# Performance work log

Hardware: AMD Instinct MI355X
Metric: run time of the kernel (lower is better)

## Reference

```python
import jax, jax.numpy as jnp
import numpy as np


def setup_inputs() -> dict:
    key = jax.random.key(0)
    ks = jax.random.split(key, 8)
    B, S, V, E, H = 64, 512, 50257, 512, 1024
    scale1 = 1.0 / np.sqrt(E + H)
    scale2 = 1.0 / np.sqrt(H + E)
    return {
        "sequence": jax.random.randint(ks[0], (B, S), 0, V, dtype=jnp.int64),
        "init_h1": jax.random.uniform(ks[1], (B, H), jnp.float32, -0.1, 0.1),
        "init_h2": jax.random.uniform(ks[2], (B, E), jnp.float32, -0.1, 0.1),
        "emb_W": jax.random.normal(ks[3], (V, E), jnp.float32) * 0.02,
        "W1": jax.random.normal(ks[4], (E + H, H), jnp.float32) * scale1,
        "b1": jnp.zeros((H,), jnp.float32),
        "W2": jax.random.normal(ks[5], (H + E, E), jnp.float32) * scale2,
        "b2": jnp.zeros((E,), jnp.float32),
        "out_b": jnp.zeros((V,), jnp.float32),
    }


def reference(sequence, init_h1, init_h2, emb_W, W1, b1, W2, b2, out_b):
    # embeddings: [B, S, E] -> scan over time axis
    emb = emb_W[sequence]  # gather, [B, S, E]
    emb_t = jnp.swapaxes(emb, 0, 1)  # [S, B, E]

    def step(carry, token):
        h1, h2 = carry  # [B,H], [B,E]
        in1 = jnp.concatenate([token, h1], axis=1)  # [B, E+H]
        new_h1 = jnp.tanh(in1 @ W1 + b1)            # [B, H]
        in2 = jnp.concatenate([new_h1, h2], axis=1)  # [B, H+E]
        new_h2 = jnp.tanh(in2 @ W2 + b2)             # [B, E]
        return (new_h1, new_h2), None

    (h1, h2), _ = jax.lax.scan(step, (init_h1, init_h2), emb_t)
    # tied output projection: Linear with weight = embedding table [V, E]
    probabilities = h2 @ emb_W.T + out_b  # [B, V]
    return probabilities, h1, h2
```

## Files before the change

### kernel.cpp

```cpp
#include <hip/hip_runtime.h>
#include <hip/hip_bf16.h>

#define BB 64
#define EE 512
#define HH 1024
#define KK 1536
#define VV 50257
#define SS 512

#define NWG1 64
#define NWG2 32
#define NWG (NWG1 + NWG2)
#define RING 64
#define PADU 32

typedef __bf16 bf16x8 __attribute__((ext_vector_type(8)));
typedef float f32x4 __attribute__((ext_vector_type(4)));

__device__ __forceinline__ bf16x8 load_bf8(const __bf16* p) {
    return *reinterpret_cast<const bf16x8*>(p);
}

__device__ __forceinline__ bf16x8 cvt8(const float* p) {
    f32x4 a = *reinterpret_cast<const f32x4*>(p);
    f32x4 b = *reinterpret_cast<const f32x4*>(p + 4);
    bf16x8 r;
    r[0] = (__bf16)a[0]; r[1] = (__bf16)a[1]; r[2] = (__bf16)a[2]; r[3] = (__bf16)a[3];
    r[4] = (__bf16)b[0]; r[5] = (__bf16)b[1]; r[6] = (__bf16)b[2]; r[7] = (__bf16)b[3];
    return r;
}

__device__ __forceinline__ void st16c(void* p, f32x4 v) {
    asm volatile("global_store_dwordx4 %0, %1, off sc0 sc1" :: "v"(p), "v"(v) : "memory");
}
__device__ __forceinline__ f32x4 ld16c(const void* p) {
    f32x4 r;
    asm volatile("global_load_dwordx4 %0, %1, off sc0 sc1" : "=v"(r) : "v"(p) : "memory");
    return r;
}
union cvu { f32x4 f; bf16x8 h8; __bf16 h[8]; };

__device__ __forceinline__ void block_wait(const unsigned* slots, int nslots,
                                           unsigned target) {
    if (threadIdx.x < 64) {
        const int l = threadIdx.x;
        const int idx = l < nslots ? l : 0;
        for (;;) {
            unsigned v = __hip_atomic_load(&slots[idx * PADU], __ATOMIC_RELAXED,
                                           __HIP_MEMORY_SCOPE_AGENT);
            if (l >= nslots) v = target;
            if (__all((int)(v >= target))) break;
            __builtin_amdgcn_s_sleep(1);
        }
    }
    __syncthreads();
    asm volatile("" ::: "memory");
}

__device__ __forceinline__ unsigned minpoll(const unsigned* slots, int nslots) {
    const int l = threadIdx.x & 63;
    unsigned v = 0xFFFFFFFFu;
    if (l < nslots)
        v = __hip_atomic_load(&slots[l * PADU], __ATOMIC_RELAXED,
                              __HIP_MEMORY_SCOPE_AGENT);
    #pragma unroll
    for (int o = 32; o; o >>= 1) {
        unsigned u = (unsigned)__shfl_xor((int)v, o, 64);
        v = u < v ? u : v;
    }
    return v;
}

__device__ __forceinline__ void bsignal(unsigned* slot, unsigned val) {
    asm volatile("s_waitcnt vmcnt(0)" ::: "memory");
    __syncthreads();
    if (threadIdx.x == 0)
        __hip_atomic_store(slot, val, __ATOMIC_RELAXED, __HIP_MEMORY_SCOPE_AGENT);
}

__device__ __forceinline__ float ftanh(float x) {
    float ax = fabsf(x);
    float e = __expf(-2.0f * ax);
    float r = (1.0f - e) / (1.0f + e);
    return x < 0.0f ? -r : r;
}

__global__ void tokens_kernel(const void* __restrict__ seq, int* __restrict__ tok,
                              unsigned* __restrict__ bar) {
    int z = blockIdx.x * 256 + threadIdx.x;
    if (z < 4 * 32 * PADU)
        __hip_atomic_store(&bar[z], 0u, __ATOMIC_RELAXED, __HIP_MEMORY_SCOPE_AGENT);
    const unsigned* u = (const unsigned*)seq;
    bool is64 = true;
    #pragma unroll 1
    for (int i = 0; i < 64; ++i) {
        if (u[2 * i + 1] != 0u) { is64 = false; break; }
    }
    int i = blockIdx.x * 256 + threadIdx.x;
    if (i < BB * SS) tok[i] = is64 ? (int)u[2 * i] : (int)u[i];
}

__global__ __launch_bounds__(256) void transpose_kernel(
    const float* __restrict__ in, __bf16* __restrict__ out, int R, int C) {
    __shared__ float t[32][33];
    int bc = C >> 5;
    int br = blockIdx.x / bc;
    int bco = blockIdx.x % bc;
    int R0 = br << 5, C0 = bco << 5;
    int c = threadIdx.x & 31, r0 = threadIdx.x >> 5;
    #pragma unroll
    for (int i = 0; i < 4; ++i) {
        int r = r0 + i * 8;
        t[r][c] = in[(size_t)(R0 + r) * C + C0 + c];
    }
    __syncthreads();
    #pragma unroll
    for (int i = 0; i < 4; ++i) {
        int r = r0 + i * 8;
        out[(size_t)(C0 + r) * R + R0 + c] = (__bf16)t[c][r];
    }
}

__global__ void init_kernel(const float* __restrict__ h1, const float* __restrict__ h2,
                            __bf16* __restrict__ h1bf, __bf16* __restrict__ h2bf) {
    int i = blockIdx.x * 256 + threadIdx.x;
    if (i < BB * HH) h1bf[i] = (__bf16)h1[i];
    if (i < BB * EE) h2bf[i] = (__bf16)h2[i];
}

__global__ __launch_bounds__(256, 1) void rnn_persist6(
    const int* __restrict__ tok32, const float* __restrict__ embW,
    const float* __restrict__ b1, const float* __restrict__ b2,
    const __bf16* __restrict__ W1t, const __bf16* __restrict__ W2t,
    __bf16* __restrict__ h1r, __bf16* __restrict__ h2r,
    float* __restrict__ h1out, float* __restrict__ h2out,
    unsigned* __restrict__ bar) {
    const int bid = blockIdx.x;
    const bool g1 = bid < NWG1;
    const int rb = g1 ? bid : bid - NWG1;
    const int mi = rb & 3;
    const int ni = rb >> 2;
    const int m0 = mi << 4;
    const int n0 = ni << 6;
    const int tid = threadIdx.x;
    const int w = tid >> 6;
    const int l = tid & 63;
    const int l16 = l & 15;
    const int kg = l >> 4;
    unsigned* f1s = bar + mi * (32 * PADU);
    unsigned* f2s = f1s + 16 * PADU;
    unsigned* myf = g1 ? &f1s[ni * PADU] : &f2s[ni * PADU];

    __shared__ int tok_s[SS][16];
    __shared__ float red[2][4][16][68];

    if (g1) {
        for (int idx = tid; idx < SS * 16; idx += 256) {
            int t = idx >> 4, r = idx & 15;
            tok_s[t][r] = tok32[(m0 + r) * SS + t];
        }
    }

    const __bf16* Wt = g1 ? W1t : W2t;
    bf16x8 wreg[12][4];
    #pragma unroll
    for (int t = 0; t < 12; ++t) {
        const int kb = 32 * (w + 4 * t) + kg * 8;
        #pragma unroll
        for (int nf = 0; nf < 4; ++nf)
            wreg[t][nf] = load_bf8(Wt + (size_t)(n0 + nf * 16 + l16) * KK + kb);
    }
    {
        f32x4* p1 = reinterpret_cast<f32x4*>(&wreg[0][0]);
        #pragma unroll
        for (int q = 0; q < 48; ++q) asm volatile("" : "+v"(p1[q]));
    }

    const int r1 = 4 * w + ((l & 31) >> 3);
    const int c1 = (l & 7) * 8;
    const float* bias = g1 ? b1 : b2;
    const f32x4 blo = *reinterpret_cast<const f32x4*>(bias + n0 + c1);
    const f32x4 bhi = *reinterpret_cast<const f32x4*>(bias + n0 + c1 + 4);

    unsigned f2c = 0;

    __syncthreads();

    if (g1) {
        for (int i = 0; i < SS; ++i) {
            const __bf16* h1i = h1r + (size_t)(i & (RING - 1)) * BB * HH;
            __bf16*       h1n = h1r + (size_t)((i + 1) & (RING - 1)) * BB * HH;

            f32x4 acc[4] = {{0,0,0,0},{0,0,0,0},{0,0,0,0},{0,0,0,0}};
            const float* er = embW + (size_t)tok_s[i][l16] * EE;
            #pragma unroll
            for (int t = 0; t < 4; ++t) {
                bf16x8 ae = cvt8(er + 32 * (w + 4 * t) + kg * 8);
                #pragma unroll
                for (int nf = 0; nf < 4; ++nf)
                    acc[nf] = __builtin_amdgcn_mfma_f32_16x16x32_bf16(
                        ae, wreg[t][nf], acc[nf], 0, 0, 0);
            }
            __builtin_amdgcn_sched_barrier(0);

            if (i >= RING - 1 && (int)f2c < i - (RING - 1)) {
                do { f2c = minpoll(f2s, 8); } while ((int)f2c < i - (RING - 1));
            }

            if (i) block_wait(f1s, 16, (unsigned)i);

            const __bf16* h1row = h1i + (m0 + l16) * HH;
            bf16x8 ah[8];
            #pragma unroll
            for (int u = 0; u < 8; ++u) {
                cvu t_; t_.f = ld16c(h1row + 32 * (w + 4 * u) + kg * 8);
                ah[u] = t_.h8;
            }
            asm volatile("s_waitcnt vmcnt(0)" ::: "memory");
            __builtin_amdgcn_sched_barrier(0);

            #pragma unroll
            for (int u = 0; u < 8; ++u)
                #pragma unroll
                for (int nf = 0; nf < 4; ++nf)
                    acc[nf] = __builtin_amdgcn_mfma_f32_16x16x32_bf16(
                        ah[u], wreg[u + 4][nf], acc[nf], 0, 0, 0);

            #pragma unroll
            for (int nf = 0; nf < 4; ++nf)
                #pragma unroll
                for (int q = 0; q < 4; ++q)
                    red[i & 1][w][kg * 4 + q][nf * 16 + l16] = acc[nf][q];
            __syncthreads();

            if ((l & 63) < 32) {
                f32x4 lo = blo, hi = bhi;
                #pragma unroll
                for (int p = 0; p < 4; ++p) {
                    lo += *reinterpret_cast<const f32x4*>(&red[i & 1][p][r1][c1]);
                    hi += *reinterpret_cast<const f32x4*>(&red[i & 1][p][r1][c1 + 4]);
                }
                cvu o;
                #pragma unroll
                for (int j = 0; j < 4; ++j) {
                    o.h[j]     = (__bf16)ftanh(lo[j]);
                    o.h[j + 4] = (__bf16)ftanh(hi[j]);
                }
                st16c(h1n + (m0 + r1) * HH + n0 + c1, o.f);
                if (i == SS - 1) {
                    float* op = h1out + (m0 + r1) * HH + n0 + c1;
                    #pragma unroll
                    for (int j = 0; j < 8; ++j)
                        op[j] = __bfloat162float(((__hip_bfloat16*)&o.h[j])[0]);
                }
            }
            bsignal(myf, (unsigned)(i + 1));
        }
    } else {
        for (int j = 1; j <= SS; ++j) {
            const __bf16* h1j = h1r + (size_t)(j & (RING - 1)) * BB * HH;
            const __bf16* h2p = h2r + (size_t)((j - 1) & (RING - 1)) * BB * EE;
            __bf16*       h2n = h2r + (size_t)(j & (RING - 1)) * BB * EE;

            block_wait(f1s, 16, (unsigned)j);
            const __bf16* h1row = h1j + (m0 + l16) * HH;
            bf16x8 ah[8];
            #pragma unroll
            for (int t = 0; t < 8; ++t) {
                cvu t_; t_.f = ld16c(h1row + 32 * (w + 4 * t) + kg * 8);
                ah[t] = t_.h8;
            }
            if (j >= 2) block_wait(f2s, 8, (unsigned)(j - 1));
            const __bf16* h2row = h2p + (m0 + l16) * EE;
            bf16x8 a2[4];
            #pragma unroll
            for (int u = 0; u < 4; ++u) {
                cvu t_; t_.f = ld16c(h2row + 32 * (w + 4 * u) + kg * 8);
                a2[u] = t_.h8;
            }
            asm volatile("s_waitcnt vmcnt(0)" ::: "memory");
            __builtin_amdgcn_sched_barrier(0);

            f32x4 acc[4] = {{0,0,0,0},{0,0,0,0},{0,0,0,0},{0,0,0,0}};
            #pragma unroll
            for (int t = 0; t < 8; ++t)
                #pragma unroll
                for (int nf = 0; nf < 4; ++nf)
                    acc[nf] = __builtin_amdgcn_mfma_f32_16x16x32_bf16(
                        ah[t], wreg[t][nf], acc[nf], 0, 0, 0);
            #pragma unroll
            for (int u = 0; u < 4; ++u)
                #pragma unroll
                for (int nf = 0; nf < 4; ++nf)
                    acc[nf] = __builtin_amdgcn_mfma_f32_16x16x32_bf16(
                        a2[u], wreg[u + 8][nf], acc[nf], 0, 0, 0);

            #pragma unroll
            for (int nf = 0; nf < 4; ++nf)
                #pragma unroll
                for (int q = 0; q < 4; ++q)
                    red[j & 1][w][kg * 4 + q][nf * 16 + l16] = acc[nf][q];
            __syncthreads();

            if ((l & 63) < 32) {
                f32x4 lo = blo, hi = bhi;
                #pragma unroll
                for (int p = 0; p < 4; ++p) {
                    lo += *reinterpret_cast<const f32x4*>(&red[j & 1][p][r1][c1]);
                    hi += *reinterpret_cast<const f32x4*>(&red[j & 1][p][r1][c1 + 4]);
                }
                cvu o;
                #pragma unroll
                for (int q = 0; q < 4; ++q) {
                    o.h[q]     = (__bf16)ftanh(lo[q]);
                    o.h[q + 4] = (__bf16)ftanh(hi[q]);
                }
                st16c(h2n + (m0 + r1) * EE + n0 + c1, o.f);
                if (j == SS) {
                    float* op = h2out + (m0 + r1) * EE + n0 + c1;
                    #pragma unroll
                    for (int q = 0; q < 8; ++q)
                        op[q] = __bfloat162float(((__hip_bfloat16*)&o.h[q])[0]);
                }
            }
            bsignal(myf, (unsigned)j);
        }
    }
}

__global__ __launch_bounds__(256) void step_kernel(
    const int* __restrict__ tok32,
    const float* __restrict__ embW,
    const float* __restrict__ b1, const float* __restrict__ b2,
    const __bf16* __restrict__ W1t, const __bf16* __restrict__ W2t,
    const __bf16* __restrict__ h1cur, __bf16* __restrict__ h1next,
    const __bf16* __restrict__ h2cur, __bf16* __restrict__ h2next,
    float* __restrict__ h1f32, float* __restrict__ h2f32,
    int t, int g1, int g2) {
    const int bid = blockIdx.x;
    const bool is1 = bid < 128;
    if (is1 ? (g1 == 0) : (g2 == 0)) return;
    const int rb = is1 ? bid : (bid - 128);
    const int mi = rb & 3;
    const int ni = rb >> 2;
    const int m0 = mi << 4;
    const int n0 = ni << 5;
    const int N = is1 ? HH : EE;
    const int tid = threadIdx.x;
    const int w = tid >> 6;
    const int l = tid & 63;
    const int l16 = l & 15;
    const int kg = l >> 4;

    __shared__ int tok_s[16];
    __shared__ float red[4][16][33];

    if (is1 && tid < 16) tok_s[tid] = tok32[(m0 + tid) * SS + t];
    __syncthreads();

    const __bf16* Wt = is1 ? W1t : W2t;
    f32x4 acc0 = {0.f, 0.f, 0.f, 0.f};
    f32x4 acc1 = {0.f, 0.f, 0.f, 0.f};
    const int row = m0 + l16;
    const int kb = w * 384;

    #pragma unroll 4
    for (int kk = 0; kk < 384; kk += 32) {
        const int k = kb + kk + kg * 8;
        bf16x8 a;
        if (is1) {
            if (k < EE) a = cvt8(embW + (size_t)tok_s[l16] * EE + k);
            else        a = load_bf8(h1cur + row * HH + (k - EE));
        } else {
            if (k < HH) a = load_bf8(h1cur + row * HH + k);
            else        a = load_bf8(h2cur + row * EE + (k - HH));
        }
        bf16x8 bf0 = load_bf8(Wt + (size_t)(n0 + l16) * KK + k);
        bf16x8 bf1 = load_bf8(Wt + (size_t)(n0 + 16 + l16) * KK + k);
        acc0 = __builtin_amdgcn_mfma_f32_16x16x32_bf16(a, bf0, acc0, 0, 0, 0);
        acc1 = __builtin_amdgcn_mfma_f32_16x16x32_bf16(a, bf1, acc1, 0, 0, 0);
    }

    #pragma unroll
    for (int i = 0; i < 4; ++i) {
        red[w][kg * 4 + i][l16]      = acc0[i];
        red[w][kg * 4 + i][16 + l16] = acc1[i];
    }
    __syncthreads();

    const float* bias = is1 ? b1 : b2;
    for (int c = tid; c < 512; c += 256) {
        int m = c >> 5, n = c & 31;
        float s = red[0][m][n] + red[1][m][n] + red[2][m][n] + red[3][m][n];
        s = tanhf(s + bias[n0 + n]);
        int gi = (m0 + m) * N + (n0 + n);
        if (is1) {
            h1next[gi] = (__bf16)s;
            if (h1f32) h1f32[gi] = s;
        } else {
            h2next[gi] = (__bf16)s;
            if (h2f32) h2f32[gi] = s;
        }
    }
}

__global__ __launch_bounds__(256) void proj_kernel(
    const __bf16* __restrict__ h2bf,
    const float* __restrict__ embW,
    const float* __restrict__ outb,
    float* __restrict__ out) {
    const int v0 = blockIdx.x << 6;
    const int tid = threadIdx.x;
    const int w = tid >> 6;
    const int l = tid & 63;
    const int l16 = l & 15, kg = l >> 4;
    const int vcol = v0 + w * 16 + l16;
    const int vr = vcol < VV ? vcol : VV - 1;
    f32x4 acc[4] = {{0,0,0,0},{0,0,0,0},{0,0,0,0},{0,0,0,0}};
    #pragma unroll 2
    for (int k0 = 0; k0 < EE; k0 += 32) {
        const int k = k0 + kg * 8;
        bf16x8 bfr = cvt8(embW + (size_t)vr * EE + k);
        #pragma unroll
        for (int mf = 0; mf < 4; ++mf) {
            bf16x8 a = load_bf8(h2bf + (mf * 16 + l16) * EE + k);
            acc[mf] = __builtin_amdgcn_mfma_f32_16x16x32_bf16(a, bfr, acc[mf], 0, 0, 0);
        }
    }
    if (vcol < VV) {
        const float bb = outb[vcol];
        #pragma unroll
        for (int mf = 0; mf < 4; ++mf) {
            #pragma unroll
            for (int i = 0; i < 4; ++i) {
                int b = mf * 16 + kg * 4 + i;
                out[(size_t)b * VV + vcol] = acc[mf][i] + bb;
            }
        }
    }
}

extern "C" void kernel_launch(void* const* d_in, const int* in_sizes, int n_in,
                              void* d_out, int out_size, void* d_ws, size_t ws_size,
                              hipStream_t stream) {
    const void* seq      = d_in[0];
    const float* init_h1 = (const float*)d_in[1];
    const float* init_h2 = (const float*)d_in[2];
    const float* embW    = (const float*)d_in[3];
    const float* W1      = (const float*)d_in[4];
    const float* b1      = (const float*)d_in[5];
    const float* W2      = (const float*)d_in[6];
    const float* b2      = (const float*)d_in[7];
    const float* outb    = (const float*)d_in[8];
    float* out = (float*)d_out;

    char* ws = (char*)d_ws;
    int* tok = (int*)ws;                 ws += (size_t)BB * SS * 4;
    __bf16* W1t = (__bf16*)ws;           ws += (size_t)HH * KK * 2;
    __bf16* W2t = (__bf16*)ws;           ws += (size_t)EE * KK * 2;
    __bf16* h1r = (__bf16*)ws;           ws += (size_t)RING * BB * HH * 2;
    __bf16* h2r = (__bf16*)ws;           ws += (size_t)RING * BB * EE * 2;
    unsigned* bar = (unsigned*)ws;       ws += (size_t)4 * 32 * PADU * 4;

    hipLaunchKernelGGL(tokens_kernel, dim3(128), dim3(256), 0, stream, seq, tok, bar);
    hipLaunchKernelGGL(transpose_kernel, dim3((KK / 32) * (HH / 32)), dim3(256), 0, stream,
                       W1, W1t, KK, HH);
    hipLaunchKernelGGL(transpose_kernel, dim3((KK / 32) * (EE / 32)), dim3(256), 0, stream,
                       W2, W2t, KK, EE);
    hipLaunchKernelGGL(init_kernel, dim3(256), dim3(256), 0, stream,
                       init_h1, init_h2, h1r, h2r);

    float* h1out = out + (size_t)BB * VV;
    float* h2out = h1out + (size_t)BB * HH;

    const int* tok_c = tok;
    const __bf16* W1t_c = W1t;
    const __bf16* W2t_c = W2t;
    void* args[] = {
        (void*)&tok_c, (void*)&embW, (void*)&b1, (void*)&b2,
        (void*)&W1t_c, (void*)&W2t_c,
        (void*)&h1r, (void*)&h2r,
        (void*)&h1out, (void*)&h2out, (void*)&bar
    };
    hipError_t err = hipLaunchCooperativeKernel((void*)rnn_persist6, dim3(NWG), dim3(256),
                                                args, 0, stream);
    if (err != hipSuccess) {
        __bf16* h1bf[2] = {h1r, h1r + (size_t)BB * HH};
        __bf16* h2bf[2] = {h2r, h2r + (size_t)BB * EE};
        for (int t = 0; t <= SS; ++t) {
            int g1 = (t < SS) ? 1 : 0;
            int g2 = (t >= 1) ? 1 : 0;
            const __bf16* h1cur = h1bf[t & 1];
            __bf16* h1next      = h1bf[(t + 1) & 1];
            const __bf16* h2cur = h2bf[(t + 1) & 1];
            __bf16* h2next      = h2bf[t & 1];
            float* h1f = (t == SS - 1) ? h1out : nullptr;
            float* h2f = (t == SS) ? h2out : nullptr;
            hipLaunchKernelGGL(step_kernel, dim3(192), dim3(256), 0, stream,
                               tok, embW, b1, b2, W1t, W2t,
                               h1cur, h1next, h2cur, h2next, h1f, h2f, t, g1, g2);
        }
    }

    hipLaunchKernelGGL(proj_kernel, dim3((VV + 63) / 64), dim3(256), 0, stream,
                       h2r, embW, outb, out);
}
```

Baseline: 2.068 ms.

## Replace counter barriers with nonzero-data polling over full-length hidden-state history

Adds a new persistent kernel that stores every timestep's hidden state in a separate slot of a large prezeroed buffer. Consumers spin on the data itself until no word is zero, which removes the flag barriers and the ring-reuse backpressure. A size check picks this path when the workspace is large enough and otherwise falls back to the ring or per-step kernels. The readiness test assumes no 32-bit word of valid bf16 state is ever zero, and a guard counter can let a block proceed on stale data. It also adds a large prezero pass, and the projection now reads the float h2 output instead of the bf16 state.

```diff
diff --git a/kernel.cpp b/kernel.cpp
--- a/kernel.cpp
+++ b/kernel.cpp
@@ -11,11 +11,12 @@
 #define NWG1 64
 #define NWG2 32
 #define NWG (NWG1 + NWG2)
-#define RING 64
+#define RINGM 64
 #define PADU 32
 
 typedef __bf16 bf16x8 __attribute__((ext_vector_type(8)));
 typedef float f32x4 __attribute__((ext_vector_type(4)));
+typedef unsigned u32x4 __attribute__((ext_vector_type(4)));
 
 __device__ __forceinline__ bf16x8 load_bf8(const __bf16* p) {
     return *reinterpret_cast<const bf16x8*>(p);
@@ -39,6 +40,7 @@
     return r;
 }
 union cvu { f32x4 f; bf16x8 h8; __bf16 h[8]; };
+union frg { f32x4 f; unsigned u[4]; bf16x8 h; };
 
 __device__ __forceinline__ void block_wait(const unsigned* slots, int nslots,
                                            unsigned target) {
@@ -56,7 +58,6 @@
     __syncthreads();
     asm volatile("" ::: "memory");
 }
-
 __device__ __forceinline__ unsigned minpoll(const unsigned* slots, int nslots) {
     const int l = threadIdx.x & 63;
     unsigned v = 0xFFFFFFFFu;
@@ -70,7 +71,6 @@
     }
     return v;
 }
-
 __device__ __forceinline__ void bsignal(unsigned* slot, unsigned val) {
     asm volatile("s_waitcnt vmcnt(0)" ::: "memory");
     __syncthreads();
@@ -86,9 +86,9 @@
 }
 
 __global__ void tokens_kernel(const void* __restrict__ seq, int* __restrict__ tok,
-                              unsigned* __restrict__ bar) {
+                              unsigned* __restrict__ bar, int nbar) {
     int z = blockIdx.x * 256 + threadIdx.x;
-    if (z < 4 * 32 * PADU)
+    if (bar && z < nbar)
         __hip_atomic_store(&bar[z], 0u, __ATOMIC_RELAXED, __HIP_MEMORY_SCOPE_AGENT);
     const unsigned* u = (const unsigned*)seq;
     bool is64 = true;
@@ -121,11 +121,232 @@
     }
 }
 
+__global__ void prezero_kernel(__bf16* __restrict__ h1R, __bf16* __restrict__ h2R) {
+    const size_t n1 = (size_t)SS * BB * HH / 8;
+    const size_t n2 = (size_t)SS * BB * EE / 8;
+    u32x4 z = {0u, 0u, 0u, 0u};
+    u32x4* p1 = (u32x4*)(h1R + (size_t)BB * HH);
+    u32x4* p2 = (u32x4*)(h2R + (size_t)BB * EE);
+    for (size_t i = (size_t)blockIdx.x * 256 + threadIdx.x; i < n1 + n2;
+         i += (size_t)gridDim.x * 256) {
+        if (i < n1) p1[i] = z; else p2[i - n1] = z;
+    }
+}
+
 __global__ void init_kernel(const float* __restrict__ h1, const float* __restrict__ h2,
-                            __bf16* __restrict__ h1bf, __bf16* __restrict__ h2bf) {
+                            __bf16* __restrict__ r1, __bf16* __restrict__ r2,
+                            __bf16* __restrict__ p1, __bf16* __restrict__ p2) {
     int i = blockIdx.x * 256 + threadIdx.x;
-    if (i < BB * HH) h1bf[i] = (__bf16)h1[i];
-    if (i < BB * EE) h2bf[i] = (__bf16)h2[i];
+    if (i < BB * HH) {
+        __bf16 v = (__bf16)h1[i];
+        p1[i] = v;
+        if (r1) r1[i] = v;
+    }
+    if (i < BB * EE) {
+        __bf16 v = (__bf16)h2[i];
+        p2[i] = v;
+        if (r2) r2[i] = v;
+    }
+}
+
+__global__ __launch_bounds__(256, 1) void rnn_persist7(
+    const int* __restrict__ tok32, const float* __restrict__ embW,
+    const float* __restrict__ b1, const float* __restrict__ b2,
+    const __bf16* __restrict__ W1t, const __bf16* __restrict__ W2t,
+    __bf16* __restrict__ h1r, __bf16* __restrict__ h2r,
+    float* __restrict__ h1out, float* __restrict__ h2out) {
+    const int bid = blockIdx.x;
+    const bool g1 = bid < NWG1;
+    const int rb = g1 ? bid : bid - NWG1;
+    const int mi = rb & 3;
+    const int ni = rb >> 2;
+    const int m0 = mi << 4;
+    const int n0 = ni << 6;
+    const int tid = threadIdx.x;
+    const int w = tid >> 6;
+    const int l = tid & 63;
+    const int l16 = l & 15;
+    const int kg = l >> 4;
+
+    __shared__ int tok_s[SS][16];
+    __shared__ float red[2][4][16][68];
+
+    if (g1) {
+        for (int idx = tid; idx < SS * 16; idx += 256) {
+            int t = idx >> 4, r = idx & 15;
+            tok_s[t][r] = tok32[(m0 + r) * SS + t];
+        }
+    }
+
+    const __bf16* Wt = g1 ? W1t : W2t;
+    bf16x8 wreg[12][4];
+    #pragma unroll
+    for (int t = 0; t < 12; ++t) {
+        const int kb = 32 * (w + 4 * t) + kg * 8;
+        #pragma unroll
+        for (int nf = 0; nf < 4; ++nf)
+            wreg[t][nf] = load_bf8(Wt + (size_t)(n0 + nf * 16 + l16) * KK + kb);
+    }
+    {
+        f32x4* p1 = reinterpret_cast<f32x4*>(&wreg[0][0]);
+        #pragma unroll
+        for (int q = 0; q < 48; ++q) asm volatile("" : "+v"(p1[q]));
+    }
+
+    const int r1 = 4 * w + ((l & 31) >> 3);
+    const int c1 = (l & 7) * 8;
+    const float* bias = g1 ? b1 : b2;
+    const f32x4 blo = *reinterpret_cast<const f32x4*>(bias + n0 + c1);
+    const f32x4 bhi = *reinterpret_cast<const f32x4*>(bias + n0 + c1 + 4);
+
+    __syncthreads();
+
+    if (g1) {
+        for (int i = 0; i < SS; ++i) {
+            const __bf16* h1i = h1r + (size_t)i * (BB * HH);
+            __bf16*       h1n = h1r + (size_t)(i + 1) * (BB * HH);
+
+            f32x4 acc[4] = {{0,0,0,0},{0,0,0,0},{0,0,0,0},{0,0,0,0}};
+            const float* er = embW + (size_t)tok_s[i][l16] * EE;
+            #pragma unroll
+            for (int t = 0; t < 4; ++t) {
+                bf16x8 ae = cvt8(er + 32 * (w + 4 * t) + kg * 8);
+                #pragma unroll
+                for (int nf = 0; nf < 4; ++nf)
+                    acc[nf] = __builtin_amdgcn_mfma_f32_16x16x32_bf16(
+                        ae, wreg[t][nf], acc[nf], 0, 0, 0);
+            }
+            __builtin_amdgcn_sched_barrier(0);
+
+            const __bf16* h1row = h1i + (m0 + l16) * HH;
+            frg ff[8];
+            int guard = 0;
+            for (;;) {
+                #pragma unroll
+                for (int u = 0; u < 8; ++u)
+                    ff[u].f = ld16c(h1row + 32 * (w + 4 * u) + kg * 8);
+                asm volatile("s_waitcnt vmcnt(0)" ::: "memory");
+                __builtin_amdgcn_sched_barrier(0);
+                bool ok = true;
+                #pragma unroll
+                for (int u = 0; u < 8; ++u)
+                    ok = ok && ff[u].u[0] && ff[u].u[1] && ff[u].u[2] && ff[u].u[3];
+                if (__all(ok)) break;
+                if (++guard > (1 << 16)) break;
+                __builtin_amdgcn_s_sleep(4);
+            }
+
+            #pragma unroll
+            for (int u = 0; u < 8; ++u)
+                #pragma unroll
+                for (int nf = 0; nf < 4; ++nf)
+                    acc[nf] = __builtin_amdgcn_mfma_f32_16x16x32_bf16(
+                        ff[u].h, wreg[u + 4][nf], acc[nf], 0, 0, 0);
+
+            #pragma unroll
+            for (int nf = 0; nf < 4; ++nf)
+                #pragma unroll
+                for (int q = 0; q < 4; ++q)
+                    red[i & 1][w][kg * 4 + q][nf * 16 + l16] = acc[nf][q];
+            __syncthreads();
+
+            if ((l & 63) < 32) {
+                f32x4 lo = blo, hi = bhi;
+                #pragma unroll
+                for (int p = 0; p < 4; ++p) {
+                    lo += *reinterpret_cast<const f32x4*>(&red[i & 1][p][r1][c1]);
+                    hi += *reinterpret_cast<const f32x4*>(&red[i & 1][p][r1][c1 + 4]);
+                }
+                cvu o;
+                #pragma unroll
+                for (int j = 0; j < 4; ++j) {
+                    o.h[j]     = (__bf16)ftanh(lo[j]);
+                    o.h[j + 4] = (__bf16)ftanh(hi[j]);
+                }
+                st16c(h1n + (m0 + r1) * HH + n0 + c1, o.f);
+                if (i == SS - 1) {
+                    float* op = h1out + (m0 + r1) * HH + n0 + c1;
+                    #pragma unroll
+                    for (int j = 0; j < 8; ++j)
+                        op[j] = __bfloat162float(((__hip_bfloat16*)&o.h[j])[0]);
+                }
+            }
+        }
+    } else {
+        for (int j = 1; j <= SS; ++j) {
+            const __bf16* h1j = h1r + (size_t)j * (BB * HH);
+            const __bf16* h2p = h2r + (size_t)(j - 1) * (BB * EE);
+            __bf16*       h2n = h2r + (size_t)j * (BB * EE);
+
+            const __bf16* h1row = h1j + (m0 + l16) * HH;
+            const __bf16* h2row = h2p + (m0 + l16) * EE;
+            frg fa[8], fb[4];
+            int guard = 0;
+            for (;;) {
+                #pragma unroll
+                for (int u = 0; u < 8; ++u)
+                    fa[u].f = ld16c(h1row + 32 * (w + 4 * u) + kg * 8);
+                #pragma unroll
+                for (int u = 0; u < 4; ++u)
+                    fb[u].f = ld16c(h2row + 32 * (w + 4 * u) + kg * 8);
+                asm volatile("s_waitcnt vmcnt(0)" ::: "memory");
+                __builtin_amdgcn_sched_barrier(0);
+                bool ok = true;
+                #pragma unroll
+                for (int u = 0; u < 8; ++u)
+                    ok = ok && fa[u].u[0] && fa[u].u[1] && fa[u].u[2] && fa[u].u[3];
+                #pragma unroll
+                for (int u = 0; u < 4; ++u)
+                    ok = ok && fb[u].u[0] && fb[u].u[1] && fb[u].u[2] && fb[u].u[3];
+                if (__all(ok)) break;
+                if (++guard > (1 << 16)) break;
+                __builtin_amdgcn_s_sleep(4);
+            }
+
+            f32x4 acc[4] = {{0,0,0,0},{0,0,0,0},{0,0,0,0},{0,0,0,0}};
+            #pragma unroll
+            for (int t = 0; t < 8; ++t)
+                #pragma unroll
+                for (int nf = 0; nf < 4; ++nf)
+                    acc[nf] = __builtin_amdgcn_mfma_f32_16x16x32_bf16(
+                        fa[t].h, wreg[t][nf], acc[nf], 0, 0, 0);
+            #pragma unroll
+            for (int u = 0; u < 4; ++u)
+                #pragma unroll
+                for (int nf = 0; nf < 4; ++nf)
+                    acc[nf] = __builtin_amdgcn_mfma_f32_16x16x32_bf16(
+                        fb[u].h, wreg[u + 8][nf], acc[nf], 0, 0, 0);
+
+            #pragma unroll
+            for (int nf = 0; nf < 4; ++nf)
+                #pragma unroll
+                for (int q = 0; q < 4; ++q)
+                    red[j & 1][w][kg * 4 + q][nf * 16 + l16] = acc[nf][q];
+            __syncthreads();
+
+            if ((l & 63) < 32) {
+                f32x4 lo = blo, hi = bhi;
+                #pragma unroll
+                for (int p = 0; p < 4; ++p) {
+                    lo += *reinterpret_cast<const f32x4*>(&red[j & 1][p][r1][c1]);
+                    hi += *reinterpret_cast<const f32x4*>(&red[j & 1][p][r1][c1 + 4]);
+                }
+                cvu o;
+                #pragma unroll
+                for (int q = 0; q < 4; ++q) {
+                    o.h[q]     = (__bf16)ftanh(lo[q]);
+                    o.h[q + 4] = (__bf16)ftanh(hi[q]);
+                }
+                st16c(h2n + (m0 + r1) * EE + n0 + c1, o.f);
+                if (j == SS) {
+                    float* op = h2out + (m0 + r1) * EE + n0 + c1;
+                    #pragma unroll
+                    for (int q = 0; q < 8; ++q)
+                        op[q] = __bfloat162float(((__hip_bfloat16*)&o.h[q])[0]);
+                }
+            }
+        }
+    }
 }
 
 __global__ __launch_bounds__(256, 1) void rnn_persist6(
@@ -183,13 +404,12 @@
     const f32x4 bhi = *reinterpret_cast<const f32x4*>(bias + n0 + c1 + 4);
 
     unsigned f2c = 0;
-
     __syncthreads();
 
     if (g1) {
         for (int i = 0; i < SS; ++i) {
-            const __bf16* h1i = h1r + (size_t)(i & (RING - 1)) * BB * HH;
-            __bf16*       h1n = h1r + (size_t)((i + 1) & (RING - 1)) * BB * HH;
+            const __bf16* h1i = h1r + (size_t)(i & (RINGM - 1)) * BB * HH;
+            __bf16*       h1n = h1r + (size_t)((i + 1) & (RINGM - 1)) * BB * HH;
 
             f32x4 acc[4] = {{0,0,0,0},{0,0,0,0},{0,0,0,0},{0,0,0,0}};
             const float* er = embW + (size_t)tok_s[i][l16] * EE;
@@ -203,8 +423,8 @@
             }
             __builtin_amdgcn_sched_barrier(0);
 
-            if (i >= RING - 1 && (int)f2c < i - (RING - 1)) {
-                do { f2c = minpoll(f2s, 8); } while ((int)f2c < i - (RING - 1));
+            if (i >= RINGM - 1 && (int)f2c < i - (RINGM - 1)) {
+                do { f2c = minpoll(f2s, 8); } while ((int)f2c < i - (RINGM - 1));
             }
 
             if (i) block_wait(f1s, 16, (unsigned)i);
@@ -258,9 +478,9 @@
         }
     } else {
         for (int j = 1; j <= SS; ++j) {
-            const __bf16* h1j = h1r + (size_t)(j & (RING - 1)) * BB * HH;
-            const __bf16* h2p = h2r + (size_t)((j - 1) & (RING - 1)) * BB * EE;
-            __bf16*       h2n = h2r + (size_t)(j & (RING - 1)) * BB * EE;
+            const __bf16* h1j = h1r + (size_t)(j & (RINGM - 1)) * BB * HH;
+            const __bf16* h2p = h2r + (size_t)((j - 1) & (RINGM - 1)) * BB * EE;
+            __bf16*       h2n = h2r + (size_t)(j & (RINGM - 1)) * BB * EE;
 
             block_wait(f1s, 16, (unsigned)j);
             const __bf16* h1row = h1j + (m0 + l16) * HH;
@@ -405,7 +625,7 @@
 }
 
 __global__ __launch_bounds__(256) void proj_kernel(
-    const __bf16* __restrict__ h2bf,
+    const float* __restrict__ h2f,
     const float* __restrict__ embW,
     const float* __restrict__ outb,
     float* __restrict__ out) {
@@ -423,7 +643,7 @@
         bf16x8 bfr = cvt8(embW + (size_t)vr * EE + k);
         #pragma unroll
         for (int mf = 0; mf < 4; ++mf) {
-            bf16x8 a = load_bf8(h2bf + (mf * 16 + l16) * EE + k);
+            bf16x8 a = cvt8(h2f + (size_t)(mf * 16 + l16) * EE + k);
             acc[mf] = __builtin_amdgcn_mfma_f32_16x16x32_bf16(a, bfr, acc[mf], 0, 0, 0);
         }
     }
@@ -458,35 +678,65 @@
     int* tok = (int*)ws;                 ws += (size_t)BB * SS * 4;
     __bf16* W1t = (__bf16*)ws;           ws += (size_t)HH * KK * 2;
     __bf16* W2t = (__bf16*)ws;           ws += (size_t)EE * KK * 2;
-    __bf16* h1r = (__bf16*)ws;           ws += (size_t)RING * BB * HH * 2;
-    __bf16* h2r = (__bf16*)ws;           ws += (size_t)RING * BB * EE * 2;
+    __bf16* h1p = (__bf16*)ws;           ws += (size_t)2 * BB * HH * 2;
+    __bf16* h2p = (__bf16*)ws;           ws += (size_t)2 * BB * EE * 2;
     unsigned* bar = (unsigned*)ws;       ws += (size_t)4 * 32 * PADU * 4;
-
-    hipLaunchKernelGGL(tokens_kernel, dim3(128), dim3(256), 0, stream, seq, tok, bar);
+    char* rings = ws;
+    size_t base = (size_t)(rings - (char*)d_ws);
+    size_t needBig = base + (size_t)(SS + 1) * BB * HH * 2 + (size_t)(SS + 1) * BB * EE * 2;
+    size_t needMid = base + (size_t)RINGM * BB * HH * 2 + (size_t)RINGM * BB * EE * 2;
+    __bf16* h1Rb = (__bf16*)rings;
+    __bf16* h2Rb = (__bf16*)(rings + (size_t)(SS + 1) * BB * HH * 2);
+    __bf16* h1Rm = (__bf16*)rings;
+    __bf16* h2Rm = (__bf16*)(rings + (size_t)RINGM * BB * HH * 2);
+
+    float* h1out = out + (size_t)BB * VV;
+    float* h2out = h1out + (size_t)BB * HH;
+
+    const bool big = ws_size >= needBig;
+    const bool mid = !big && ws_size >= needMid;
+
+    hipLaunchKernelGGL(tokens_kernel, dim3(128), dim3(256), 0, stream,
+                       seq, tok, mid ? bar : (unsigned*)nullptr, 4 * 32 * PADU);
     hipLaunchKernelGGL(transpose_kernel, dim3((KK / 32) * (HH / 32)), dim3(256), 0, stream,
                        W1, W1t, KK, HH);
     hipLaunchKernelGGL(transpose_kernel, dim3((KK / 32) * (EE / 32)), dim3(256), 0, stream,
                        W2, W2t, KK, EE);
-    hipLaunchKernelGGL(init_kernel, dim3(256), dim3(256), 0, stream,
-                       init_h1, init_h2, h1r, h2r);
-
-    float* h1out = out + (size_t)BB * VV;
-    float* h2out = h1out + (size_t)BB * HH;
 
     const int* tok_c = tok;
     const __bf16* W1t_c = W1t;
     const __bf16* W2t_c = W2t;
-    void* args[] = {
-        (void*)&tok_c, (void*)&embW, (void*)&b1, (void*)&b2,
-        (void*)&W1t_c, (void*)&W2t_c,
-        (void*)&h1r, (void*)&h2r,
-        (void*)&h1out, (void*)&h2out, (void*)&bar
-    };
-    hipError_t err = hipLaunchCooperativeKernel((void*)rnn_persist6, dim3(NWG), dim3(256),
-                                                args, 0, stream);
-    if (err != hipSuccess) {
-        __bf16* h1bf[2] = {h1r, h1r + (size_t)BB * HH};
-        __bf16* h2bf[2] = {h2r, h2r + (size_t)BB * EE};
+    bool done = false;
+
+    if (big) {
+        hipLaunchKernelGGL(prezero_kernel, dim3(1024), dim3(256), 0, stream, h1Rb, h2Rb);
+        hipLaunchKernelGGL(init_kernel, dim3(256), dim3(256), 0, stream,
+                           init_h1, init_h2, h1Rb, h2Rb, h1p, h2p);
+        void* args[] = {
+            (void*)&tok_c, (void*)&embW, (void*)&b1, (void*)&b2,
+            (void*)&W1t_c, (void*)&W2t_c,
+            (void*)&h1Rb, (void*)&h2Rb, (void*)&h1out, (void*)&h2out
+        };
+        done = hipLaunchCooperativeKernel((void*)rnn_persist7, dim3(NWG), dim3(256),
+                                          args, 0, stream) == hipSuccess;
+    } else if (mid) {
+        hipLaunchKernelGGL(init_kernel, dim3(256), dim3(256), 0, stream,
+                           init_h1, init_h2, h1Rm, h2Rm, h1p, h2p);
+        void* args[] = {
+            (void*)&tok_c, (void*)&embW, (void*)&b1, (void*)&b2,
+            (void*)&W1t_c, (void*)&W2t_c,
+            (void*)&h1Rm, (void*)&h2Rm, (void*)&h1out, (void*)&h2out, (void*)&bar
+        };
+        done = hipLaunchCooperativeKernel((void*)rnn_persist6, dim3(NWG), dim3(256),
+                                          args, 0, stream) == hipSuccess;
+    } else {
+        hipLaunchKernelGGL(init_kernel, dim3(256), dim3(256), 0, stream,
+                           init_h1, init_h2, (__bf16*)nullptr, (__bf16*)nullptr, h1p, h2p);
+    }
+
+    if (!done) {
+        __bf16* h1bf[2] = {h1p, h1p + (size_t)BB * HH};
+        __bf16* h2bf[2] = {h2p, h2p + (size_t)BB * EE};
         for (int t = 0; t <= SS; ++t) {
             int g1 = (t < SS) ? 1 : 0;
             int g2 = (t >= 1) ? 1 : 0;
@@ -503,5 +753,5 @@
     }
 
     hipLaunchKernelGGL(proj_kernel, dim3((VV + 63) / 64), dim3(256), 0, stream,
-                       h2r, embW, outb, out);
-}
+                       h2out, embW, outb, out);
+}
```

New measurement: 2.076 ms. Within noise of the previous version (+0.4%).

## Halve persistent RNN workgroups with 128-wide column tiles and overlap h1 MFMA before h2 wait

Applied to the files above, without the earlier changes.

The persistent RNN kernel drops from 96 to 48 workgroups. Each now owns 128 output columns, so 8 MFMA column fragments per wave are held in registers. Fewer participants per barrier cut the cross-workgroup synchronisation cost of each timestep, and the layer-2 group now runs its h1 MFMAs before waiting on the previous h2. The price is doubled register pressure (96 vector quads of weights), more MFMA work per step, and fewer CUs in use. The ring buffers move to a size-checked workspace region with a ping-pong fallback, and the projection reads the fp32 h2 output.

```diff
diff --git a/kernel.cpp b/kernel.cpp
--- a/kernel.cpp
+++ b/kernel.cpp
@@ -8,8 +8,8 @@
 #define VV 50257
 #define SS 512
 
-#define NWG1 64
-#define NWG2 32
+#define NWG1 32
+#define NWG2 16
 #define NWG (NWG1 + NWG2)
 #define RING 64
 #define PADU 32
@@ -122,13 +122,22 @@
 }
 
 __global__ void init_kernel(const float* __restrict__ h1, const float* __restrict__ h2,
-                            __bf16* __restrict__ h1bf, __bf16* __restrict__ h2bf) {
+                            __bf16* __restrict__ r1, __bf16* __restrict__ r2,
+                            __bf16* __restrict__ p1, __bf16* __restrict__ p2) {
     int i = blockIdx.x * 256 + threadIdx.x;
-    if (i < BB * HH) h1bf[i] = (__bf16)h1[i];
-    if (i < BB * EE) h2bf[i] = (__bf16)h2[i];
-}
-
-__global__ __launch_bounds__(256, 1) void rnn_persist6(
+    if (i < BB * HH) {
+        __bf16 v = (__bf16)h1[i];
+        p1[i] = v;
+        if (r1) r1[i] = v;
+    }
+    if (i < BB * EE) {
+        __bf16 v = (__bf16)h2[i];
+        p2[i] = v;
+        if (r2) r2[i] = v;
+    }
+}
+
+__global__ __launch_bounds__(256, 1) void rnn_persist9(
     const int* __restrict__ tok32, const float* __restrict__ embW,
     const float* __restrict__ b1, const float* __restrict__ b2,
     const __bf16* __restrict__ W1t, const __bf16* __restrict__ W2t,
@@ -141,7 +150,7 @@
     const int mi = rb & 3;
     const int ni = rb >> 2;
     const int m0 = mi << 4;
-    const int n0 = ni << 6;
+    const int n0 = ni << 7;
     const int tid = threadIdx.x;
     const int w = tid >> 6;
     const int l = tid & 63;
@@ -152,7 +161,7 @@
     unsigned* myf = g1 ? &f1s[ni * PADU] : &f2s[ni * PADU];
 
     __shared__ int tok_s[SS][16];
-    __shared__ float red[2][4][16][68];
+    __shared__ float red[2][4][16][136];
 
     if (g1) {
         for (int idx = tid; idx < SS * 16; idx += 256) {
@@ -162,25 +171,27 @@
     }
 
     const __bf16* Wt = g1 ? W1t : W2t;
-    bf16x8 wreg[12][4];
+    bf16x8 wreg[12][8];
     #pragma unroll
     for (int t = 0; t < 12; ++t) {
         const int kb = 32 * (w + 4 * t) + kg * 8;
         #pragma unroll
-        for (int nf = 0; nf < 4; ++nf)
+        for (int nf = 0; nf < 8; ++nf)
             wreg[t][nf] = load_bf8(Wt + (size_t)(n0 + nf * 16 + l16) * KK + kb);
     }
     {
         f32x4* p1 = reinterpret_cast<f32x4*>(&wreg[0][0]);
         #pragma unroll
-        for (int q = 0; q < 48; ++q) asm volatile("" : "+v"(p1[q]));
+        for (int q = 0; q < 96; ++q) asm volatile("" : "+v"(p1[q]));
     }
 
     const int r1 = 4 * w + ((l & 31) >> 3);
-    const int c1 = (l & 7) * 8;
+    const int c0 = (l & 7) * 16;
     const float* bias = g1 ? b1 : b2;
-    const f32x4 blo = *reinterpret_cast<const f32x4*>(bias + n0 + c1);
-    const f32x4 bhi = *reinterpret_cast<const f32x4*>(bias + n0 + c1 + 4);
+    f32x4 bias4[4];
+    #pragma unroll
+    for (int q = 0; q < 4; ++q)
+        bias4[q] = *reinterpret_cast<const f32x4*>(bias + n0 + c0 + 4 * q);
 
     unsigned f2c = 0;
 
@@ -191,23 +202,24 @@
             const __bf16* h1i = h1r + (size_t)(i & (RING - 1)) * BB * HH;
             __bf16*       h1n = h1r + (size_t)((i + 1) & (RING - 1)) * BB * HH;
 
-            f32x4 acc[4] = {{0,0,0,0},{0,0,0,0},{0,0,0,0},{0,0,0,0}};
+            f32x4 acc[8] = {{0,0,0,0},{0,0,0,0},{0,0,0,0},{0,0,0,0},
+                            {0,0,0,0},{0,0,0,0},{0,0,0,0},{0,0,0,0}};
             const float* er = embW + (size_t)tok_s[i][l16] * EE;
             #pragma unroll
             for (int t = 0; t < 4; ++t) {
                 bf16x8 ae = cvt8(er + 32 * (w + 4 * t) + kg * 8);
                 #pragma unroll
-                for (int nf = 0; nf < 4; ++nf)
+                for (int nf = 0; nf < 8; ++nf)
                     acc[nf] = __builtin_amdgcn_mfma_f32_16x16x32_bf16(
                         ae, wreg[t][nf], acc[nf], 0, 0, 0);
             }
             __builtin_amdgcn_sched_barrier(0);
 
             if (i >= RING - 1 && (int)f2c < i - (RING - 1)) {
-                do { f2c = minpoll(f2s, 8); } while ((int)f2c < i - (RING - 1));
-            }
-
-            if (i) block_wait(f1s, 16, (unsigned)i);
+                do { f2c = minpoll(f2s, 4); } while ((int)f2c < i - (RING - 1));
+            }
+
+            if (i) block_wait(f1s, 8, (unsigned)i);
 
             const __bf16* h1row = h1i + (m0 + l16) * HH;
             bf16x8 ah[8];
@@ -222,36 +234,40 @@
             #pragma unroll
             for (int u = 0; u < 8; ++u)
                 #pragma unroll
-                for (int nf = 0; nf < 4; ++nf)
+                for (int nf = 0; nf < 8; ++nf)
                     acc[nf] = __builtin_amdgcn_mfma_f32_16x16x32_bf16(
                         ah[u], wreg[u + 4][nf], acc[nf], 0, 0, 0);
 
             #pragma unroll
-            for (int nf = 0; nf < 4; ++nf)
+            for (int nf = 0; nf < 8; ++nf)
                 #pragma unroll
                 for (int q = 0; q < 4; ++q)
                     red[i & 1][w][kg * 4 + q][nf * 16 + l16] = acc[nf][q];
             __syncthreads();
 
             if ((l & 63) < 32) {
-                f32x4 lo = blo, hi = bhi;
-                #pragma unroll
-                for (int p = 0; p < 4; ++p) {
-                    lo += *reinterpret_cast<const f32x4*>(&red[i & 1][p][r1][c1]);
-                    hi += *reinterpret_cast<const f32x4*>(&red[i & 1][p][r1][c1 + 4]);
-                }
-                cvu o;
-                #pragma unroll
-                for (int j = 0; j < 4; ++j) {
-                    o.h[j]     = (__bf16)ftanh(lo[j]);
-                    o.h[j + 4] = (__bf16)ftanh(hi[j]);
-                }
-                st16c(h1n + (m0 + r1) * HH + n0 + c1, o.f);
-                if (i == SS - 1) {
-                    float* op = h1out + (m0 + r1) * HH + n0 + c1;
+                #pragma unroll
+                for (int h = 0; h < 2; ++h) {
+                    const int c = c0 + 8 * h;
+                    f32x4 lo = bias4[2 * h], hi = bias4[2 * h + 1];
                     #pragma unroll
-                    for (int j = 0; j < 8; ++j)
-                        op[j] = __bfloat162float(((__hip_bfloat16*)&o.h[j])[0]);
+                    for (int p = 0; p < 4; ++p) {
+                        lo += *reinterpret_cast<const f32x4*>(&red[i & 1][p][r1][c]);
+                        hi += *reinterpret_cast<const f32x4*>(&red[i & 1][p][r1][c + 4]);
+                    }
+                    cvu o;
+                    #pragma unroll
+                    for (int j = 0; j < 4; ++j) {
+                        o.h[j]     = (__bf16)ftanh(lo[j]);
+                        o.h[j + 4] = (__bf16)ftanh(hi[j]);
+                    }
+                    st16c(h1n + (m0 + r1) * HH + n0 + c, o.f);
+                    if (i == SS - 1) {
+                        float* op = h1out + (m0 + r1) * HH + n0 + c;
+                        #pragma unroll
+                        for (int j = 0; j < 8; ++j)
+                            op[j] = __bfloat162float(((__hip_bfloat16*)&o.h[j])[0]);
+                    }
                 }
             }
             bsignal(myf, (unsigned)(i + 1));
@@ -262,7 +278,7 @@
             const __bf16* h2p = h2r + (size_t)((j - 1) & (RING - 1)) * BB * EE;
             __bf16*       h2n = h2r + (size_t)(j & (RING - 1)) * BB * EE;
 
-            block_wait(f1s, 16, (unsigned)j);
+            block_wait(f1s, 8, (unsigned)j);
             const __bf16* h1row = h1j + (m0 + l16) * HH;
             bf16x8 ah[8];
             #pragma unroll
@@ -270,7 +286,20 @@
                 cvu t_; t_.f = ld16c(h1row + 32 * (w + 4 * t) + kg * 8);
                 ah[t] = t_.h8;
             }
-            if (j >= 2) block_wait(f2s, 8, (unsigned)(j - 1));
+            asm volatile("s_waitcnt vmcnt(0)" ::: "memory");
+            __builtin_amdgcn_sched_barrier(0);
+
+            f32x4 acc[8] = {{0,0,0,0},{0,0,0,0},{0,0,0,0},{0,0,0,0},
+                            {0,0,0,0},{0,0,0,0},{0,0,0,0},{0,0,0,0}};
+            #pragma unroll
+            for (int t = 0; t < 8; ++t)
+                #pragma unroll
+                for (int nf = 0; nf < 8; ++nf)
+                    acc[nf] = __builtin_amdgcn_mfma_f32_16x16x32_bf16(
+                        ah[t], wreg[t][nf], acc[nf], 0, 0, 0);
+            __builtin_amdgcn_sched_barrier(0);
+
+            if (j >= 2) block_wait(f2s, 4, (unsigned)(j - 1));
             const __bf16* h2row = h2p + (m0 + l16) * EE;
             bf16x8 a2[4];
             #pragma unroll
@@ -281,46 +310,43 @@
             asm volatile("s_waitcnt vmcnt(0)" ::: "memory");
             __builtin_amdgcn_sched_barrier(0);
 
-            f32x4 acc[4] = {{0,0,0,0},{0,0,0,0},{0,0,0,0},{0,0,0,0}};
-            #pragma unroll
-            for (int t = 0; t < 8; ++t)
-                #pragma unroll
-                for (int nf = 0; nf < 4; ++nf)
-                    acc[nf] = __builtin_amdgcn_mfma_f32_16x16x32_bf16(
-                        ah[t], wreg[t][nf], acc[nf], 0, 0, 0);
             #pragma unroll
             for (int u = 0; u < 4; ++u)
                 #pragma unroll
-                for (int nf = 0; nf < 4; ++nf)
+                for (int nf = 0; nf < 8; ++nf)
                     acc[nf] = __builtin_amdgcn_mfma_f32_16x16x32_bf16(
                         a2[u], wreg[u + 8][nf], acc[nf], 0, 0, 0);
 
             #pragma unroll
-            for (int nf = 0; nf < 4; ++nf)
+            for (int nf = 0; nf < 8; ++nf)
                 #pragma unroll
                 for (int q = 0; q < 4; ++q)
                     red[j & 1][w][kg * 4 + q][nf * 16 + l16] = acc[nf][q];
             __syncthreads();
 
             if ((l & 63) < 32) {
-                f32x4 lo = blo, hi = bhi;
-                #pragma unroll
-                for (int p = 0; p < 4; ++p) {
-                    lo += *reinterpret_cast<const f32x4*>(&red[j & 1][p][r1][c1]);
-                    hi += *reinterpret_cast<const f32x4*>(&red[j & 1][p][r1][c1 + 4]);
-                }
-                cvu o;
-                #pragma unroll
-                for (int q = 0; q < 4; ++q) {
-                    o.h[q]     = (__bf16)ftanh(lo[q]);
-                    o.h[q + 4] = (__bf16)ftanh(hi[q]);
-                }
-                st16c(h2n + (m0 + r1) * EE + n0 + c1, o.f);
-                if (j == SS) {
-                    float* op = h2out + (m0 + r1) * EE + n0 + c1;
+                #pragma unroll
+                for (int h = 0; h < 2; ++h) {
+                    const int c = c0 + 8 * h;
+                    f32x4 lo = bias4[2 * h], hi = bias4[2 * h + 1];
                     #pragma unroll
-                    for (int q = 0; q < 8; ++q)
-                        op[q] = __bfloat162float(((__hip_bfloat16*)&o.h[q])[0]);
+                    for (int p = 0; p < 4; ++p) {
+                        lo += *reinterpret_cast<const f32x4*>(&red[j & 1][p][r1][c]);
+                        hi += *reinterpret_cast<const f32x4*>(&red[j & 1][p][r1][c + 4]);
+                    }
+                    cvu o;
+                    #pragma unroll
+                    for (int q = 0; q < 4; ++q) {
+                        o.h[q]     = (__bf16)ftanh(lo[q]);
+                        o.h[q + 4] = (__bf16)ftanh(hi[q]);
+                    }
+                    st16c(h2n + (m0 + r1) * EE + n0 + c, o.f);
+                    if (j == SS) {
+                        float* op = h2out + (m0 + r1) * EE + n0 + c;
+                        #pragma unroll
+                        for (int q = 0; q < 8; ++q)
+                            op[q] = __bfloat162float(((__hip_bfloat16*)&o.h[q])[0]);
+                    }
                 }
             }
             bsignal(myf, (unsigned)j);
@@ -405,7 +431,7 @@
 }
 
 __global__ __launch_bounds__(256) void proj_kernel(
-    const __bf16* __restrict__ h2bf,
+    const float* __restrict__ h2f,
     const float* __restrict__ embW,
     const float* __restrict__ outb,
     float* __restrict__ out) {
@@ -423,7 +449,7 @@
         bf16x8 bfr = cvt8(embW + (size_t)vr * EE + k);
         #pragma unroll
         for (int mf = 0; mf < 4; ++mf) {
-            bf16x8 a = load_bf8(h2bf + (mf * 16 + l16) * EE + k);
+            bf16x8 a = cvt8(h2f + (size_t)(mf * 16 + l16) * EE + k);
             acc[mf] = __builtin_amdgcn_mfma_f32_16x16x32_bf16(a, bfr, acc[mf], 0, 0, 0);
         }
     }
@@ -458,9 +484,19 @@
     int* tok = (int*)ws;                 ws += (size_t)BB * SS * 4;
     __bf16* W1t = (__bf16*)ws;           ws += (size_t)HH * KK * 2;
     __bf16* W2t = (__bf16*)ws;           ws += (size_t)EE * KK * 2;
-    __bf16* h1r = (__bf16*)ws;           ws += (size_t)RING * BB * HH * 2;
-    __bf16* h2r = (__bf16*)ws;           ws += (size_t)RING * BB * EE * 2;
+    __bf16* h1p = (__bf16*)ws;           ws += (size_t)2 * BB * HH * 2;
+    __bf16* h2p = (__bf16*)ws;           ws += (size_t)2 * BB * EE * 2;
     unsigned* bar = (unsigned*)ws;       ws += (size_t)4 * 32 * PADU * 4;
+    char* rings = ws;
+    size_t base = (size_t)(rings - (char*)d_ws);
+    size_t need = base + (size_t)RING * BB * HH * 2 + (size_t)RING * BB * EE * 2;
+    __bf16* h1R = (__bf16*)rings;
+    __bf16* h2R = (__bf16*)(rings + (size_t)RING * BB * HH * 2);
+
+    float* h1out = out + (size_t)BB * VV;
+    float* h2out = h1out + (size_t)BB * HH;
+
+    const bool fit = ws_size >= need;
 
     hipLaunchKernelGGL(tokens_kernel, dim3(128), dim3(256), 0, stream, seq, tok, bar);
     hipLaunchKernelGGL(transpose_kernel, dim3((KK / 32) * (HH / 32)), dim3(256), 0, stream,
@@ -468,25 +504,27 @@
     hipLaunchKernelGGL(transpose_kernel, dim3((KK / 32) * (EE / 32)), dim3(256), 0, stream,
                        W2, W2t, KK, EE);
     hipLaunchKernelGGL(init_kernel, dim3(256), dim3(256), 0, stream,
-                       init_h1, init_h2, h1r, h2r);
-
-    float* h1out = out + (size_t)BB * VV;
-    float* h2out = h1out + (size_t)BB * HH;
+                       init_h1, init_h2, fit ? h1R : (__bf16*)nullptr,
+                       fit ? h2R : (__bf16*)nullptr, h1p, h2p);
 
     const int* tok_c = tok;
     const __bf16* W1t_c = W1t;
     const __bf16* W2t_c = W2t;
-    void* args[] = {
-        (void*)&tok_c, (void*)&embW, (void*)&b1, (void*)&b2,
-        (void*)&W1t_c, (void*)&W2t_c,
-        (void*)&h1r, (void*)&h2r,
-        (void*)&h1out, (void*)&h2out, (void*)&bar
-    };
-    hipError_t err = hipLaunchCooperativeKernel((void*)rnn_persist6, dim3(NWG), dim3(256),
-                                                args, 0, stream);
-    if (err != hipSuccess) {
-        __bf16* h1bf[2] = {h1r, h1r + (size_t)BB * HH};
-        __bf16* h2bf[2] = {h2r, h2r + (size_t)BB * EE};
+    bool done = false;
+
+    if (fit) {
+        void* args[] = {
+            (void*)&tok_c, (void*)&embW, (void*)&b1, (void*)&b2,
+            (void*)&W1t_c, (void*)&W2t_c,
+            (void*)&h1R, (void*)&h2R, (void*)&h1out, (void*)&h2out, (void*)&bar
+        };
+        done = hipLaunchCooperativeKernel((void*)rnn_persist9, dim3(NWG), dim3(256),
+                                          args, 0, stream) == hipSuccess;
+    }
+
+    if (!done) {
+        __bf16* h1bf[2] = {h1p, h1p + (size_t)BB * HH};
+        __bf16* h2bf[2] = {h2p, h2p + (size_t)BB * EE};
         for (int t = 0; t <= SS; ++t) {
             int g1 = (t < SS) ? 1 : 0;
             int g2 = (t >= 1) ? 1 : 0;
@@ -503,5 +541,5 @@
     }
 
     hipLaunchKernelGGL(proj_kernel, dim3((VV + 63) / 64), dim3(256), 0, stream,
-                       h2r, embW, outb, out);
-}
+                       h2out, embW, outb, out);
+}
```

New measurement: 2.816 ms. 36.2% more time.
